# Optimization experiments

Hardware: AMD Instinct MI355X
Metric: run time of the kernel (lower is better)

Reference implementation:

```python
import jax, jax.numpy as jnp
import numpy as np

B = 262144
IN, H = 2, 50


def setup_inputs() -> dict:
    key = jax.random.key(0)
    ks = jax.random.split(key, 12)
    k = 1.0 / np.sqrt(H)
    u = lambda kk, shape: jax.random.uniform(kk, shape, jnp.float32, -k, k)
    return {
        "s": jax.random.normal(ks[0], (B, IN), jnp.float32),
        "h": jax.random.normal(ks[1], (B, H), jnp.float32),
        "w_ih": u(ks[2], (3 * H, IN)),
        "w_hh": u(ks[3], (3 * H, H)),
        "b_ih": u(ks[4], (3 * H,)),
        "b_hh": u(ks[5], (3 * H,)),
        "actor_w": u(ks[6], (2, H)),
        "actor_b": u(ks[7], (2,)),
        "critic_w": u(ks[8], (1, H)),
        "critic_b": u(ks[9], (1,)),
    }


def reference(s, h, w_ih, w_hh, b_ih, b_hh, actor_w, actor_b, critic_w, critic_b):
    # PyTorch GRUCell gate math (gate order: reset, update, new)
    gi = s @ w_ih.T + b_ih          # [B, 3H]
    gh = h @ w_hh.T + b_hh          # [B, 3H]
    i_r, i_z, i_n = jnp.split(gi, 3, axis=1)
    h_r, h_z, h_n = jnp.split(gh, 3, axis=1)
    r = jax.nn.sigmoid(i_r + h_r)
    z = jax.nn.sigmoid(i_z + h_z)
    n = jnp.tanh(i_n + r * h_n)
    h_new = (1.0 - z) * n + z * h   # [B, H]
    c = h_new @ critic_w.T + critic_b            # [B, 1]
    pi = jax.nn.softmax(h_new @ actor_w.T + actor_b, axis=1)  # [B, 2]
    return h_new, c, pi
```

## Files before the change

### kernel.cpp

```cpp
#include <hip/hip_runtime.h>


#define BDIM 256

typedef __bf16 bf16x8 __attribute__((ext_vector_type(8)));
typedef float f32x4 __attribute__((ext_vector_type(4)));

__device__ __forceinline__ float bf2f(unsigned short u) {
    union { unsigned u; float f; } x; x.u = ((unsigned)u) << 16; return x.f;
}
__device__ __forceinline__ unsigned short f2bf(float f) {
    union { float f; unsigned u; } x; x.f = f;
    unsigned r = x.u + 0x7fffu + ((x.u >> 16) & 1u);
    return (unsigned short)(r >> 16);
}
__device__ __forceinline__ unsigned packbf(float a, float b) {
    return (unsigned)f2bf(a) | ((unsigned)f2bf(b) << 16);
}

__global__ __launch_bounds__(BDIM, 4) void gru_fused(
    const float* __restrict__ s,
    const float* __restrict__ h,
    const float* __restrict__ w_ih,
    const float* __restrict__ w_hh,
    const float* __restrict__ b_ih,
    const float* __restrict__ b_hh,
    const float* __restrict__ actor_w,
    const float* __restrict__ actor_b,
    const float* __restrict__ critic_w,
    const float* __restrict__ critic_b,
    float* __restrict__ out,
    int Btot, int nTiles)
{
    __shared__ __align__(16) unsigned short xlds[64 * 72];
    __shared__ __align__(16) unsigned short wlds[1536 * 8];
    __shared__ float sflds[64 * 2];
    __shared__ float awc[152];
    __shared__ float win0l[64], win1l[64], binl[64];

    const int tid  = threadIdx.x;
    const int wave = tid >> 6;
    const int lane = tid & 63;
    const int c16  = lane & 15;
    const int quad = lane >> 4;

    for (int e = tid; e < 1536; e += BDIM) {
        int ln = e & 63;
        int ks = (e >> 6) & 1;
        int t  = (e >> 7) & 3;
        int g  = e >> 9;
        int n  = t * 16 + (ln & 15);
        int kbase = ks * 32 + (ln >> 4) * 8;
        unsigned short vals[8];
        if (n < 50) {
            int r = g * 50 + n;
            #pragma unroll
            for (int i = 0; i < 8; ++i) {
                int k = kbase + i;
                float v = 0.f;
                if (k < 50)       v = w_hh[r * 50 + k];
                else if (k == 50) v = (g < 2) ? w_ih[r * 2 + 0] : 0.f;
                else if (k == 51) v = (g < 2) ? w_ih[r * 2 + 1] : 0.f;
                else if (k == 52) {
                    v = b_hh[r];
                    if (g < 2) v += b_ih[r];
                }
                vals[i] = f2bf(v);
            }
        } else {
            #pragma unroll
            for (int i = 0; i < 8; ++i) vals[i] = 0;
        }
        #pragma unroll
        for (int i = 0; i < 8; ++i) wlds[e * 8 + i] = vals[i];
    }
    for (int k = tid; k < 152; k += BDIM) {
        float v = 0.f;
        if (k < 100)      v = actor_w[k];
        else if (k < 150) v = critic_w[k - 100];
        awc[k] = v;
    }
    if (tid < 64) {
        int j = tid;
        float w0 = 0.f, w1 = 0.f, bb = 0.f;
        if (j < 50) {
            w0 = w_ih[(100 + j) * 2 + 0];
            w1 = w_ih[(100 + j) * 2 + 1];
            bb = b_ih[100 + j];
        }
        win0l[j] = w0; win1l[j] = w1; binl[j] = bb;
    }
    const float ab0 = actor_b[0], ab1 = actor_b[1], cb = critic_b[0];

    const float2* h2 = (const float2*)h;
    const float2* s2 = (const float2*)s;
    unsigned* xlds32 = (unsigned*)xlds;
    float2* out2 = (float2*)out;
    const long long outc_off   = (long long)Btot * 50;
    const long long outpi2_off = ((long long)Btot * 51) >> 1;

    float2 pf[7];
    int bt = blockIdx.x;
    {
        int rb = bt * 64;
        #pragma unroll
        for (int j = 0; j < 7; ++j) {
            int d = tid + j * 256;
            if (d < 1600)       pf[j] = h2[rb * 25 + d];
            else if (d < 1664)  pf[j] = s2[rb + (d - 1600)];
        }
    }

    while (bt < nTiles) {
        const int rowbase = bt * 64;
        __syncthreads();
        #pragma unroll
        for (int j = 0; j < 7; ++j) {
            int d = tid + j * 256;
            if (d < 1600) {
                int r = d / 25, dk = d - r * 25;
                xlds32[r * 36 + dk] = packbf(pf[j].x, pf[j].y);
            } else if (d < 1664) {
                int r = d - 1600;
                sflds[r * 2 + 0] = pf[j].x;
                sflds[r * 2 + 1] = pf[j].y;
                xlds32[r * 36 + 25] = packbf(pf[j].x, pf[j].y);
            }
        }
        if (tid < 64) {
            xlds32[tid * 36 + 26] = 0x00003f80u;
            #pragma unroll
            for (int q = 27; q < 32; ++q) xlds32[tid * 36 + q] = 0u;
        }
        __syncthreads();

        const int nbt = bt + gridDim.x;
        {
            int pb = (nbt < nTiles) ? nbt : bt;
            int rb = pb * 64;
            #pragma unroll
            for (int j = 0; j < 7; ++j) {
                int d = tid + j * 256;
                if (d < 1600)       pf[j] = h2[rb * 25 + d];
                else if (d < 1664)  pf[j] = s2[rb + (d - 1600)];
            }
        }

        const unsigned short* arow = &xlds[(wave * 16 + c16) * 72 + quad * 8];
        bf16x8 a0 = *(const bf16x8*)(arow);
        bf16x8 a1 = *(const bf16x8*)(arow + 32);
        f32x4 acc[3][4];
        #pragma unroll
        for (int g = 0; g < 3; ++g) {
            #pragma unroll
            for (int t = 0; t < 4; ++t) {
                f32x4 a = {0.f, 0.f, 0.f, 0.f};
                const unsigned short* wb = &wlds[(((g * 4 + t) * 2) * 64 + lane) * 8];
                bf16x8 b0 = *(const bf16x8*)(wb);
                bf16x8 b1 = *(const bf16x8*)(wb + 64 * 8);
                a = __builtin_amdgcn_mfma_f32_16x16x32_bf16(a0, b0, a, 0, 0, 0);
                a = __builtin_amdgcn_mfma_f32_16x16x32_bf16(a1, b1, a, 0, 0, 0);
                acc[g][t] = a;
            }
        }

        #pragma unroll
        for (int reg = 0; reg < 4; ++reg) {
            int lr = wave * 16 + quad * 4 + reg;
            float s0 = sflds[lr * 2 + 0];
            float s1 = sflds[lr * 2 + 1];
            #pragma unroll
            for (int t = 0; t < 4; ++t) {
                int j = t * 16 + c16;
                float pr = acc[0][t][reg];
                float pz = acc[1][t][reg];
                float hn = acc[2][t][reg];
                float inn = fmaf(s1, win1l[j], fmaf(s0, win0l[j], binl[j]));
                float rg = __builtin_amdgcn_rcpf(1.f + __expf(-pr));
                float zg = __builtin_amdgcn_rcpf(1.f + __expf(-pz));
                float x = inn + rg * hn;
                x = fminf(fmaxf(x, -20.f), 20.f);
                float e2 = __expf(2.f * x);
                float ng = (e2 - 1.f) * __builtin_amdgcn_rcpf(e2 + 1.f);
                if (j < 50) {
                    float hv = bf2f(xlds[lr * 72 + j]);
                    float hnew = (1.f - zg) * ng + zg * hv;
                    out[(long long)(rowbase + lr) * 50 + j] = hnew;
                    xlds[lr * 72 + j] = f2bf(hnew);
                }
            }
        }
        __syncthreads();

        {
            int row = wave * 16 + (lane >> 2);
            int sub = lane & 3;
            int kn = (sub == 3) ? 11 : 13;
            float a0p = 0.f, a1p = 0.f, ccp = 0.f;
            #pragma unroll
            for (int i = 0; i < 13; ++i) {
                int k = sub * 13 + i;
                float hv = (i < kn) ? bf2f(xlds[row * 72 + k]) : 0.f;
                a0p = fmaf(hv, awc[k],       a0p);
                a1p = fmaf(hv, awc[50 + k],  a1p);
                ccp = fmaf(hv, awc[100 + k], ccp);
            }
            a0p += __shfl_xor(a0p, 1); a0p += __shfl_xor(a0p, 2);
            a1p += __shfl_xor(a1p, 1); a1p += __shfl_xor(a1p, 2);
            ccp += __shfl_xor(ccp, 1); ccp += __shfl_xor(ccp, 2);
            if (sub == 0) {
                int gr = rowbase + row;
                float A0 = a0p + ab0, A1 = a1p + ab1;
                out[outc_off + gr] = ccp + cb;
                float m = fmaxf(A0, A1);
                float e0 = __expf(A0 - m), e1 = __expf(A1 - m);
                float inv = 1.f / (e0 + e1);
                float2 pv; pv.x = e0 * inv; pv.y = e1 * inv;
                out2[outpi2_off + gr] = pv;
            }
        }
        bt = nbt;
    }
}

extern "C" void kernel_launch(void* const* d_in, const int* in_sizes, int n_in,
                              void* d_out, int out_size, void* d_ws, size_t ws_size,
                              hipStream_t stream) {
    const float* s        = (const float*)d_in[0];
    const float* h        = (const float*)d_in[1];
    const float* w_ih     = (const float*)d_in[2];
    const float* w_hh     = (const float*)d_in[3];
    const float* b_ih     = (const float*)d_in[4];
    const float* b_hh     = (const float*)d_in[5];
    const float* actor_w  = (const float*)d_in[6];
    const float* actor_b  = (const float*)d_in[7];
    const float* critic_w = (const float*)d_in[8];
    const float* critic_b = (const float*)d_in[9];
    float* out = (float*)d_out;

    int Btot = in_sizes[1] / 50;
    int nTiles = Btot / 64;
    int grid = nTiles < 1024 ? nTiles : 1024;

    gru_fused<<<grid, BDIM, 0, stream>>>(s, h, w_ih, w_hh, b_ih, b_hh,
                                         actor_w, actor_b, critic_w, critic_b,
                                         out, Btot, nTiles);
}
```

Measured before the change: 143.4 us.

## Make each wave own its 16-row tile and drop block-wide barriers

Each wave now loads, packs and stores its own 16 rows of h and s into LDS, so the per-tile __syncthreads barriers go away and waves run independently. The actor and critic heads are computed straight from the MFMA accumulator registers with 16-lane shuffle reductions, replacing the separate LDS pass. Small weight vectors move from LDS into registers, and the static padding columns are written once at startup. The trade-offs are more registers per thread and correctness that depends on wave-local LDS ordering, enforced only by a compiler memory fence.

```diff
diff --git a/kernel.cpp b/kernel.cpp
--- a/kernel.cpp
+++ b/kernel.cpp
@@ -1,10 +1,13 @@
 #include <hip/hip_runtime.h>
+#include <hip/hip_bf16.h>
 
 
 #define BDIM 256
 
 typedef __bf16 bf16x8 __attribute__((ext_vector_type(8)));
 typedef float f32x4 __attribute__((ext_vector_type(4)));
+typedef unsigned __attribute__((may_alias)) u32a;
+typedef unsigned short __attribute__((may_alias)) u16a;
 
 __device__ __forceinline__ float bf2f(unsigned short u) {
     union { unsigned u; float f; } x; x.u = ((unsigned)u) << 16; return x.f;
@@ -15,7 +18,12 @@
     return (unsigned short)(r >> 16);
 }
 __device__ __forceinline__ unsigned packbf(float a, float b) {
-    return (unsigned)f2bf(a) | ((unsigned)f2bf(b) << 16);
+    union { __hip_bfloat162 h; unsigned u; } c;
+    c.h = __float22bfloat162_rn(make_float2(a, b));
+    return c.u;
+}
+__device__ __forceinline__ bf16x8 ldsfrag(const unsigned short* p) {
+    bf16x8 v; __builtin_memcpy(&v, p, 16); return v;
 }
 
 __global__ __launch_bounds__(BDIM, 4) void gru_fused(
@@ -34,15 +42,18 @@
 {
     __shared__ __align__(16) unsigned short xlds[64 * 72];
     __shared__ __align__(16) unsigned short wlds[1536 * 8];
-    __shared__ float sflds[64 * 2];
-    __shared__ float awc[152];
-    __shared__ float win0l[64], win1l[64], binl[64];
 
     const int tid  = threadIdx.x;
     const int wave = tid >> 6;
     const int lane = tid & 63;
     const int c16  = lane & 15;
     const int quad = lane >> 4;
+    const int R    = wave * 16;
+
+    u32a* xlds32 = (u32a*)xlds;
+
+    for (int i = tid; i < 2304; i += BDIM)
+        xlds32[i] = ((i % 36) == 26) ? 0x00003f80u : 0u;
 
     for (int e = tid; e < 1536; e += BDIM) {
         int ln = e & 63;
@@ -74,150 +85,144 @@
         #pragma unroll
         for (int i = 0; i < 8; ++i) wlds[e * 8 + i] = vals[i];
     }
-    for (int k = tid; k < 152; k += BDIM) {
-        float v = 0.f;
-        if (k < 100)      v = actor_w[k];
-        else if (k < 150) v = critic_w[k - 100];
-        awc[k] = v;
-    }
-    if (tid < 64) {
-        int j = tid;
-        float w0 = 0.f, w1 = 0.f, bb = 0.f;
-        if (j < 50) {
-            w0 = w_ih[(100 + j) * 2 + 0];
-            w1 = w_ih[(100 + j) * 2 + 1];
-            bb = b_ih[100 + j];
-        }
-        win0l[j] = w0; win1l[j] = w1; binl[j] = bb;
+
+    float wi0[4], wi1[4], bi[4], aw0[4], aw1[4], awc[4];
+    #pragma unroll
+    for (int t = 0; t < 4; ++t) {
+        int j = t * 16 + c16;
+        bool ok = (j < 50);
+        wi0[t] = ok ? w_ih[(100 + j) * 2 + 0] : 0.f;
+        wi1[t] = ok ? w_ih[(100 + j) * 2 + 1] : 0.f;
+        bi[t]  = ok ? b_ih[100 + j]           : 0.f;
+        aw0[t] = ok ? actor_w[j]              : 0.f;
+        aw1[t] = ok ? actor_w[50 + j]         : 0.f;
+        awc[t] = ok ? critic_w[j]             : 0.f;
     }
     const float ab0 = actor_b[0], ab1 = actor_b[1], cb = critic_b[0];
+
+    __syncthreads();
 
     const float2* h2 = (const float2*)h;
     const float2* s2 = (const float2*)s;
-    unsigned* xlds32 = (unsigned*)xlds;
-    float2* out2 = (float2*)out;
-    const long long outc_off   = (long long)Btot * 50;
-    const long long outpi2_off = ((long long)Btot * 51) >> 1;
+    const long long outc = (long long)Btot * 50;
+    float2* opi = (float2*)(out + (long long)Btot * 51);
 
     float2 pf[7];
     int bt = blockIdx.x;
     {
-        int rb = bt * 64;
-        #pragma unroll
-        for (int j = 0; j < 7; ++j) {
-            int d = tid + j * 256;
-            if (d < 1600)       pf[j] = h2[rb * 25 + d];
-            else if (d < 1664)  pf[j] = s2[rb + (d - 1600)];
-        }
+        long long hb = (long long)(bt * 64 + R) * 25;
+        #pragma unroll
+        for (int j = 0; j < 6; ++j) pf[j] = h2[hb + lane + j * 64];
+        if (lane < 16)      pf[6] = h2[hb + 384 + lane];
+        else if (lane < 32) pf[6] = s2[bt * 64 + R + lane - 16];
     }
 
     while (bt < nTiles) {
         const int rowbase = bt * 64;
-        __syncthreads();
-        #pragma unroll
-        for (int j = 0; j < 7; ++j) {
-            int d = tid + j * 256;
-            if (d < 1600) {
-                int r = d / 25, dk = d - r * 25;
-                xlds32[r * 36 + dk] = packbf(pf[j].x, pf[j].y);
-            } else if (d < 1664) {
-                int r = d - 1600;
-                sflds[r * 2 + 0] = pf[j].x;
-                sflds[r * 2 + 1] = pf[j].y;
-                xlds32[r * 36 + 25] = packbf(pf[j].x, pf[j].y);
-            }
-        }
-        if (tid < 64) {
-            xlds32[tid * 36 + 26] = 0x00003f80u;
-            #pragma unroll
-            for (int q = 27; q < 32; ++q) xlds32[tid * 36 + q] = 0u;
-        }
-        __syncthreads();
+
+        #pragma unroll
+        for (int j = 0; j < 6; ++j) {
+            int d = lane + j * 64;
+            int r = d / 25, dk = d - r * 25;
+            xlds32[(R + r) * 36 + dk] = packbf(pf[j].x, pf[j].y);
+        }
+        if (lane < 16)
+            xlds32[(R + 15) * 36 + 9 + lane] = packbf(pf[6].x, pf[6].y);
+        else if (lane < 32)
+            xlds32[(R + lane - 16) * 36 + 25] = packbf(pf[6].x, pf[6].y);
+
+        asm volatile("" ::: "memory");
 
         const int nbt = bt + gridDim.x;
         {
             int pb = (nbt < nTiles) ? nbt : bt;
-            int rb = pb * 64;
-            #pragma unroll
-            for (int j = 0; j < 7; ++j) {
-                int d = tid + j * 256;
-                if (d < 1600)       pf[j] = h2[rb * 25 + d];
-                else if (d < 1664)  pf[j] = s2[rb + (d - 1600)];
-            }
-        }
-
-        const unsigned short* arow = &xlds[(wave * 16 + c16) * 72 + quad * 8];
-        bf16x8 a0 = *(const bf16x8*)(arow);
-        bf16x8 a1 = *(const bf16x8*)(arow + 32);
-        f32x4 acc[3][4];
-        #pragma unroll
-        for (int g = 0; g < 3; ++g) {
-            #pragma unroll
-            for (int t = 0; t < 4; ++t) {
-                f32x4 a = {0.f, 0.f, 0.f, 0.f};
-                const unsigned short* wb = &wlds[(((g * 4 + t) * 2) * 64 + lane) * 8];
-                bf16x8 b0 = *(const bf16x8*)(wb);
-                bf16x8 b1 = *(const bf16x8*)(wb + 64 * 8);
-                a = __builtin_amdgcn_mfma_f32_16x16x32_bf16(a0, b0, a, 0, 0, 0);
-                a = __builtin_amdgcn_mfma_f32_16x16x32_bf16(a1, b1, a, 0, 0, 0);
-                acc[g][t] = a;
-            }
-        }
-
-        #pragma unroll
-        for (int reg = 0; reg < 4; ++reg) {
-            int lr = wave * 16 + quad * 4 + reg;
-            float s0 = sflds[lr * 2 + 0];
-            float s1 = sflds[lr * 2 + 1];
-            #pragma unroll
-            for (int t = 0; t < 4; ++t) {
-                int j = t * 16 + c16;
-                float pr = acc[0][t][reg];
-                float pz = acc[1][t][reg];
-                float hn = acc[2][t][reg];
-                float inn = fmaf(s1, win1l[j], fmaf(s0, win0l[j], binl[j]));
-                float rg = __builtin_amdgcn_rcpf(1.f + __expf(-pr));
-                float zg = __builtin_amdgcn_rcpf(1.f + __expf(-pz));
-                float x = inn + rg * hn;
+            long long hb = (long long)(pb * 64 + R) * 25;
+            #pragma unroll
+            for (int j = 0; j < 6; ++j) pf[j] = h2[hb + lane + j * 64];
+            if (lane < 16)      pf[6] = h2[hb + 384 + lane];
+            else if (lane < 32) pf[6] = s2[pb * 64 + R + lane - 16];
+        }
+
+        float2 srow[4];
+        #pragma unroll
+        for (int reg = 0; reg < 4; ++reg)
+            srow[reg] = s2[rowbase + R + quad * 4 + reg];
+
+        const unsigned short* arow = &xlds[(R + c16) * 72 + quad * 8];
+        bf16x8 a0 = ldsfrag(arow);
+        bf16x8 a1 = ldsfrag(arow + 32);
+
+        float hn_r[4][4];
+        #pragma unroll
+        for (int t = 0; t < 4; ++t) {
+            f32x4 ar = {0.f,0.f,0.f,0.f}, az = ar, an = ar;
+            const int tb = (t * 128 + lane) * 8;
+            bf16x8 br0 = ldsfrag(&wlds[tb]);
+            bf16x8 br1 = ldsfrag(&wlds[tb + 512]);
+            bf16x8 bz0 = ldsfrag(&wlds[tb + 4096]);
+            bf16x8 bz1 = ldsfrag(&wlds[tb + 4608]);
+            bf16x8 bn0 = ldsfrag(&wlds[tb + 8192]);
+            bf16x8 bn1 = ldsfrag(&wlds[tb + 8704]);
+            ar = __builtin_amdgcn_mfma_f32_16x16x32_bf16(a0, br0, ar, 0, 0, 0);
+            ar = __builtin_amdgcn_mfma_f32_16x16x32_bf16(a1, br1, ar, 0, 0, 0);
+            az = __builtin_amdgcn_mfma_f32_16x16x32_bf16(a0, bz0, az, 0, 0, 0);
+            az = __builtin_amdgcn_mfma_f32_16x16x32_bf16(a1, bz1, az, 0, 0, 0);
+            an = __builtin_amdgcn_mfma_f32_16x16x32_bf16(a0, bn0, an, 0, 0, 0);
+            an = __builtin_amdgcn_mfma_f32_16x16x32_bf16(a1, bn1, an, 0, 0, 0);
+
+            int j = t * 16 + c16;
+            #pragma unroll
+            for (int reg = 0; reg < 4; ++reg) {
+                int lr = R + quad * 4 + reg;
+                float inn = fmaf(srow[reg].y, wi1[t],
+                            fmaf(srow[reg].x, wi0[t], bi[t]));
+                float rg = __builtin_amdgcn_rcpf(1.f + __expf(-ar[reg]));
+                float zg = __builtin_amdgcn_rcpf(1.f + __expf(-az[reg]));
+                float x = inn + rg * an[reg];
                 x = fminf(fmaxf(x, -20.f), 20.f);
                 float e2 = __expf(2.f * x);
                 float ng = (e2 - 1.f) * __builtin_amdgcn_rcpf(e2 + 1.f);
-                if (j < 50) {
-                    float hv = bf2f(xlds[lr * 72 + j]);
-                    float hnew = (1.f - zg) * ng + zg * hv;
-                    out[(long long)(rowbase + lr) * 50 + j] = hnew;
-                    xlds[lr * 72 + j] = f2bf(hnew);
-                }
-            }
-        }
-        __syncthreads();
-
-        {
-            int row = wave * 16 + (lane >> 2);
-            int sub = lane & 3;
-            int kn = (sub == 3) ? 11 : 13;
-            float a0p = 0.f, a1p = 0.f, ccp = 0.f;
-            #pragma unroll
-            for (int i = 0; i < 13; ++i) {
-                int k = sub * 13 + i;
-                float hv = (i < kn) ? bf2f(xlds[row * 72 + k]) : 0.f;
-                a0p = fmaf(hv, awc[k],       a0p);
-                a1p = fmaf(hv, awc[50 + k],  a1p);
-                ccp = fmaf(hv, awc[100 + k], ccp);
-            }
-            a0p += __shfl_xor(a0p, 1); a0p += __shfl_xor(a0p, 2);
-            a1p += __shfl_xor(a1p, 1); a1p += __shfl_xor(a1p, 2);
-            ccp += __shfl_xor(ccp, 1); ccp += __shfl_xor(ccp, 2);
-            if (sub == 0) {
-                int gr = rowbase + row;
-                float A0 = a0p + ab0, A1 = a1p + ab1;
-                out[outc_off + gr] = ccp + cb;
-                float m = fmaxf(A0, A1);
-                float e0 = __expf(A0 - m), e1 = __expf(A1 - m);
-                float inv = 1.f / (e0 + e1);
-                float2 pv; pv.x = e0 * inv; pv.y = e1 * inv;
-                out2[outpi2_off + gr] = pv;
-            }
+                float hv = bf2f(((const u16a*)xlds)[lr * 72 + j]);
+                float hnew = (1.f - zg) * ng + zg * hv;
+                bool ok = (j < 50);
+                hn_r[reg][t] = ok ? hnew : 0.f;
+                if (ok) out[(long long)(rowbase + lr) * 50 + j] = hnew;
+            }
+        }
+
+        float sum0[4], sum1[4], sumc[4];
+        #pragma unroll
+        for (int reg = 0; reg < 4; ++reg) {
+            float p0 = 0.f, p1 = 0.f, pc = 0.f;
+            #pragma unroll
+            for (int t = 0; t < 4; ++t) {
+                p0 = fmaf(hn_r[reg][t], aw0[t], p0);
+                p1 = fmaf(hn_r[reg][t], aw1[t], p1);
+                pc = fmaf(hn_r[reg][t], awc[t], pc);
+            }
+            #pragma unroll
+            for (int m = 1; m < 16; m <<= 1) {
+                p0 += __shfl_xor(p0, m);
+                p1 += __shfl_xor(p1, m);
+                pc += __shfl_xor(pc, m);
+            }
+            sum0[reg] = p0; sum1[reg] = p1; sumc[reg] = pc;
+        }
+        if (c16 < 4) {
+            float A0 = (c16 == 0) ? sum0[0] : (c16 == 1) ? sum0[1]
+                     : (c16 == 2) ? sum0[2] : sum0[3];
+            float A1 = (c16 == 0) ? sum1[0] : (c16 == 1) ? sum1[1]
+                     : (c16 == 2) ? sum1[2] : sum1[3];
+            float C  = (c16 == 0) ? sumc[0] : (c16 == 1) ? sumc[1]
+                     : (c16 == 2) ? sumc[2] : sumc[3];
+            int gr = rowbase + R + quad * 4 + c16;
+            out[outc + gr] = C + cb;
+            A0 += ab0; A1 += ab1;
+            float m = fmaxf(A0, A1);
+            float e0 = __expf(A0 - m), e1 = __expf(A1 - m);
+            float inv = 1.f / (e0 + e1);
+            float2 pv; pv.x = e0 * inv; pv.y = e1 * inv;
+            opi[gr] = pv;
         }
         bt = nbt;
     }
```

Measured after the change: 142.5 us. No clear change (-0.6%).
